# Performance work log

Measured on AMD Instinct MI355X. Metric: run time of the kernel, lower is better.

The kernel has to match this reference:

```python
import jax, jax.numpy as jnp
import numpy as np

N_NODES = 20000
N_EDGES = 320000
N_FEAT = 128
MLP_HID = 64
N_GRAPHS = 16
N_LAYERS = 5
EPS = 1e-5


def setup_inputs() -> dict:
    key = jax.random.key(0)
    ks = jax.random.split(key, 8)
    x = jax.random.normal(ks[0], (N_NODES, N_FEAT), dtype=jnp.float32)
    edge_index = jax.random.randint(ks[1], (2, N_EDGES), 0, N_NODES, dtype=jnp.int64)
    batch = jnp.sort(jax.random.randint(ks[2], (N_NODES,), 0, N_GRAPHS, dtype=jnp.int64))
    W1 = jax.random.normal(ks[3], (N_LAYERS, N_FEAT, MLP_HID), dtype=jnp.float32) * 0.05
    b1 = jnp.zeros((N_LAYERS, MLP_HID), dtype=jnp.float32)
    W2 = jax.random.normal(ks[4], (N_LAYERS, MLP_HID, N_FEAT), dtype=jnp.float32) * 0.05
    b2 = jnp.zeros((N_LAYERS, N_FEAT), dtype=jnp.float32)
    gn_weight = jnp.ones((N_LAYERS, N_FEAT), dtype=jnp.float32)
    gn_bias = jnp.zeros((N_LAYERS, N_FEAT), dtype=jnp.float32)
    gn_scale = jnp.ones((N_LAYERS, N_FEAT), dtype=jnp.float32)
    lin_w = jax.random.normal(ks[5], (N_FEAT, 1), dtype=jnp.float32) * 0.05
    lin_b = jnp.zeros((1,), dtype=jnp.float32)
    return {"x": x, "edge_index": edge_index, "batch": batch,
            "W1": W1, "b1": b1, "W2": W2, "b2": b2,
            "gn_weight": gn_weight, "gn_bias": gn_bias, "gn_scale": gn_scale,
            "lin_w": lin_w, "lin_b": lin_b}


def _conv(h, src, dst, W1, b1, W2, b2):
    # message MLP is per-source-node, so compute MLP(x) once per node,
    # then gather by src and scatter-add to dst. Self loops add m[i] at i.
    m = jax.nn.relu(h @ W1 + b1) @ W2 + b2  # [N, C]
    return jax.ops.segment_sum(m[src], dst, num_segments=N_NODES) + m


def _graph_norm(h, batch, cnt, w, b, a):
    mean = jax.ops.segment_sum(h, batch, num_segments=N_GRAPHS) / cnt  # [G, C]
    out = h - a * mean[batch]
    var = jax.ops.segment_sum(out * out, batch, num_segments=N_GRAPHS) / cnt
    out = out * jax.lax.rsqrt(var[batch] + EPS)
    return w * out + b


def reference(x, edge_index, batch, W1, b1, W2, b2, gn_weight, gn_bias, gn_scale, lin_w, lin_b):
    src, dst = edge_index[0], edge_index[1]
    cnt = jax.ops.segment_sum(jnp.ones((N_NODES, 1), x.dtype), batch,
                              num_segments=N_GRAPHS)
    cnt = jnp.maximum(cnt, 1.0)  # [G, 1]
    h = x
    for i in range(N_LAYERS):
        g = _conv(h, src, dst, W1[i], b1[i], W2[i], b2[i])
        g = _graph_norm(g, batch, cnt, gn_weight[i], gn_bias[i], gn_scale[i])
        g = jax.nn.relu(g)  # dropout is identity in eval mode
        h = g if i == 0 else g + h  # residual from layer 2 onward
    pooled = jax.ops.segment_sum(h, batch, num_segments=N_GRAPHS) / cnt  # [G, C]
    return pooled @ lin_w + lin_b  # [G, 1]
```

## Files before the change

### kernel.cpp

```cpp
#include <hip/hip_runtime.h>

#define N_NODES 20000
#define N_EDGES 320000
#define N_FEAT 128
#define MLP_HID 64
#define N_GRAPHS 16
#define N_LAYERS 5
#define EPS 1e-5f

typedef __attribute__((ext_vector_type(8))) short short8;
typedef __attribute__((ext_vector_type(4))) float f32x4;

__device__ inline float bf2f(unsigned short u) { return __uint_as_float(((unsigned)u) << 16); }
__device__ inline unsigned short f2bf(float f) {
  unsigned u = __float_as_uint(f);
  u += 0x7FFF + ((u >> 16) & 1);
  return (unsigned short)(u >> 16);
}


__global__ __launch_bounds__(256) void k_deg(const int* __restrict__ dst, int* __restrict__ deg) {
  int e = blockIdx.x * 256 + threadIdx.x;
  atomicAdd(&deg[dst[e]], 1);
}

__global__ __launch_bounds__(1024) void k_scan(const int* __restrict__ deg, int* __restrict__ rowptr,
                                               int* __restrict__ cursor, const int* __restrict__ batch,
                                               float* __restrict__ cntf, float* __restrict__ pooled) {
  __shared__ int sdata[1024];
  __shared__ int spos[17];
  constexpr int CH = 20;
  int t = threadIdx.x;
  for (int i = t; i < N_GRAPHS * N_FEAT; i += 1024) pooled[i] = 0.0f;
  int base = t * CH;
  int loc[CH];
  int partial = 0;
#pragma unroll
  for (int i = 0; i < CH; i++) {
    int idx = base + i;
    int v = (idx < N_NODES) ? deg[idx] : 0;
    loc[i] = v;
    partial += v;
  }
  sdata[t] = partial;
  __syncthreads();
  for (int off = 1; off < 1024; off <<= 1) {
    int v = (t >= off) ? sdata[t - off] : 0;
    __syncthreads();
    sdata[t] += v;
    __syncthreads();
  }
  int run = sdata[t] - partial;
#pragma unroll
  for (int i = 0; i < CH; i++) {
    int idx = base + i;
    if (idx < N_NODES) {
      rowptr[idx] = run;
      cursor[idx] = run;
      run += loc[i];
    }
  }
  if (t == 1023) rowptr[N_NODES] = sdata[1023];
  if (t < 17) {
    int lo = 0, hi = N_NODES;
    while (lo < hi) {
      int mid = (lo + hi) >> 1;
      if (batch[mid] < t) lo = mid + 1; else hi = mid;
    }
    spos[t] = lo;
  }
  __syncthreads();
  if (t < N_GRAPHS) cntf[t] = fmaxf((float)(spos[t + 1] - spos[t]), 1.0f);
}

__global__ __launch_bounds__(256) void k_fill(const int* __restrict__ src, const int* __restrict__ dst,
                                              int* __restrict__ cursor, unsigned short* __restrict__ src_sorted) {
  int e = blockIdx.x * 256 + threadIdx.x;
  int d = dst[e];
  int p = atomicAdd(&cursor[d], 1);
  src_sorted[p] = (unsigned short)src[e];
}


__global__ __launch_bounds__(256) void k_prep(const float* __restrict__ W1, const float* __restrict__ W2,
                                              unsigned short* __restrict__ w1t, unsigned short* __restrict__ w2t) {
  int idx = blockIdx.x * 256 + threadIdx.x;
  if (idx < 40960) {
    int l = idx >> 13, rem = idx & 8191;
    int n = rem >> 7, k = rem & 127;
    w1t[idx] = f2bf(W1[l * 8192 + k * 64 + n]);
  } else {
    int j = idx - 40960;
    int l = j >> 13, rem = j & 8191;
    int n = rem >> 6, k = rem & 63;
    w2t[j] = f2bf(W2[l * 8192 + k * 128 + n]);
  }
}


#define PADK 136
#define PADH 72

__global__ __launch_bounds__(256) void k_mlp(const float* __restrict__ hin, unsigned short* __restrict__ mout,
                                             const unsigned short* __restrict__ w1t,
                                             const unsigned short* __restrict__ w2t,
                                             const float* __restrict__ b1, const float* __restrict__ b2) {
  __shared__ __align__(16) short hS[64 * PADK];
  __shared__ __align__(16) short w1S[64 * PADK];
  __shared__ __align__(16) short hidS[64 * PADH];
  __shared__ __align__(16) short w2S[128 * PADH];
  __shared__ float b1S[64];
  __shared__ float b2S[128];
  int t = threadIdx.x;
  int r0 = blockIdx.x * 64;
#pragma unroll
  for (int i = 0; i < 8; i++) {
    int idx = t + i * 256;
    int row = idx >> 5, c4 = idx & 31;
    float4 v = (r0 + row < N_NODES) ? ((const float4*)hin)[(size_t)(r0 + row) * 32 + c4]
                                    : make_float4(0.f, 0.f, 0.f, 0.f);
    ushort4 s;
    s.x = f2bf(v.x); s.y = f2bf(v.y); s.z = f2bf(v.z); s.w = f2bf(v.w);
    *(ushort4*)&hS[row * PADK + c4 * 4] = s;
  }
#pragma unroll
  for (int i = 0; i < 4; i++) {
    int idx = t + i * 256;
    *(int4*)&w1S[(idx >> 4) * PADK + (idx & 15) * 8] = ((const int4*)w1t)[idx];
    *(int4*)&w2S[(idx >> 3) * PADH + (idx & 7) * 8] = ((const int4*)w2t)[idx];
  }
  if (t < 64) b1S[t] = b1[t];
  else if (t < 192) b2S[t - 64] = b2[t - 64];
  __syncthreads();

  int w = t >> 6, lane = t & 63, lm = lane & 15, quad = lane >> 4;
  int mrow = w * 16 + lm;
  int orow = w * 16 + quad * 4;

  f32x4 zero = {0.f, 0.f, 0.f, 0.f};
  f32x4 acc[4] = {zero, zero, zero, zero};
#pragma unroll
  for (int k0 = 0; k0 < 128; k0 += 32) {
    short8 a = *(const short8*)&hS[mrow * PADK + k0 + quad * 8];
#pragma unroll
    for (int nt = 0; nt < 4; nt++) {
      short8 b = *(const short8*)&w1S[(nt * 16 + lm) * PADK + k0 + quad * 8];
      acc[nt] = __builtin_amdgcn_mfma_f32_16x16x32_bf16(a, b, acc[nt], 0, 0, 0);
    }
  }
#pragma unroll
  for (int nt = 0; nt < 4; nt++) {
    int col = nt * 16 + lm;
    float bb = b1S[col];
#pragma unroll
    for (int r = 0; r < 4; r++)
      hidS[(orow + r) * PADH + col] = (short)f2bf(fmaxf(acc[nt][r] + bb, 0.0f));
  }
  __syncthreads();

  f32x4 acc2[8] = {zero, zero, zero, zero, zero, zero, zero, zero};
#pragma unroll
  for (int k0 = 0; k0 < 64; k0 += 32) {
    short8 a = *(const short8*)&hidS[mrow * PADH + k0 + quad * 8];
#pragma unroll
    for (int nt = 0; nt < 8; nt++) {
      short8 b = *(const short8*)&w2S[(nt * 16 + lm) * PADH + k0 + quad * 8];
      acc2[nt] = __builtin_amdgcn_mfma_f32_16x16x32_bf16(a, b, acc2[nt], 0, 0, 0);
    }
  }
#pragma unroll
  for (int nt = 0; nt < 8; nt++) {
    int col = nt * 16 + lm;
    float bb = b2S[col];
#pragma unroll
    for (int r = 0; r < 4; r++)
      hS[(orow + r) * PADK + col] = (short)f2bf(acc2[nt][r] + bb);
  }
  __syncthreads();
#pragma unroll
  for (int i = 0; i < 4; i++) {
    int idx = t + i * 256;
    int row = idx >> 4, cc = idx & 15;
    if (r0 + row < N_NODES)
      ((int4*)mout)[(size_t)(r0 + row) * 16 + cc] = *(const int4*)&hS[row * PADK + cc * 8];
  }
}


__global__ __launch_bounds__(256) void k_scatter(const unsigned short* __restrict__ mbf, float* __restrict__ g,
                                                 const int* __restrict__ rowptr,
                                                 const unsigned short* __restrict__ srcs,
                                                 float* __restrict__ s1, float* __restrict__ s2) {
  if (blockIdx.x == 0) {
    for (int i = threadIdx.x; i < N_GRAPHS * N_FEAT; i += 256) { s1[i] = 0.0f; s2[i] = 0.0f; }
  }
  int node = (blockIdx.x * 256 + threadIdx.x) >> 6;
  int lane = threadIdx.x & 63;
  int quarter = lane >> 4;
  int q16 = lane & 15;
  const float4* m4 = (const float4*)mbf;
  float acc[8];
  union BU { float4 f; unsigned short u[8]; };
  if (quarter == 0) {
    BU U; U.f = m4[(size_t)node * 16 + q16];
#pragma unroll
    for (int j = 0; j < 8; j++) acc[j] = bf2f(U.u[j]);
  } else {
#pragma unroll
    for (int j = 0; j < 8; j++) acc[j] = 0.0f;
  }
  int e = rowptr[node], e1 = rowptr[node + 1];
  for (; e + 16 <= e1; e += 16) {
    int i0 = srcs[e + quarter];
    int i1 = srcs[e + 4 + quarter];
    int i2 = srcs[e + 8 + quarter];
    int i3 = srcs[e + 12 + quarter];
    BU U0, U1, U2, U3;
    U0.f = m4[(size_t)i0 * 16 + q16];
    U1.f = m4[(size_t)i1 * 16 + q16];
    U2.f = m4[(size_t)i2 * 16 + q16];
    U3.f = m4[(size_t)i3 * 16 + q16];
#pragma unroll
    for (int j = 0; j < 8; j++)
      acc[j] += (bf2f(U0.u[j]) + bf2f(U1.u[j])) + (bf2f(U2.u[j]) + bf2f(U3.u[j]));
  }
  for (; e + 4 <= e1; e += 4) {
    BU U0; U0.f = m4[(size_t)srcs[e + quarter] * 16 + q16];
#pragma unroll
    for (int j = 0; j < 8; j++) acc[j] += bf2f(U0.u[j]);
  }
  if (e + quarter < e1) {
    BU U0; U0.f = m4[(size_t)srcs[e + quarter] * 16 + q16];
#pragma unroll
    for (int j = 0; j < 8; j++) acc[j] += bf2f(U0.u[j]);
  }
#pragma unroll
  for (int j = 0; j < 8; j++) {
    acc[j] += __shfl_xor(acc[j], 16);
    acc[j] += __shfl_xor(acc[j], 32);
  }
  if (quarter == 0) {
    float4* g4 = (float4*)(g + (size_t)node * 128 + q16 * 8);
    g4[0] = make_float4(acc[0], acc[1], acc[2], acc[3]);
    g4[1] = make_float4(acc[4], acc[5], acc[6], acc[7]);
  }
}


#define STAT_CHUNK 8

__global__ __launch_bounds__(128) void k_stats(const float* __restrict__ in, const int* __restrict__ batch,
                                               float* __restrict__ s1, float* __restrict__ s2) {
  int n0 = blockIdx.x * STAT_CHUNK;
  int c = threadIdx.x;
  int curg = batch[n0];
  float a1 = 0.0f, a2 = 0.0f;
#pragma unroll
  for (int k = 0; k < STAT_CHUNK; k++) {
    int n = n0 + k;
    int gg = batch[n];
    if (gg != curg) {
      atomicAdd(&s1[curg * 128 + c], a1);
      atomicAdd(&s2[curg * 128 + c], a2);
      a1 = 0.0f; a2 = 0.0f;
      curg = gg;
    }
    float v = in[(size_t)n * 128 + c];
    a1 += v;
    a2 += v * v;
  }
  atomicAdd(&s1[curg * 128 + c], a1);
  atomicAdd(&s2[curg * 128 + c], a2);
}

__global__ __launch_bounds__(128) void k_segsum(const float* __restrict__ in, const int* __restrict__ batch,
                                                float* __restrict__ outbuf) {
  int n0 = blockIdx.x * STAT_CHUNK;
  int c = threadIdx.x;
  int curg = batch[n0];
  float acc = 0.0f;
#pragma unroll
  for (int k = 0; k < STAT_CHUNK; k++) {
    int n = n0 + k;
    int gg = batch[n];
    if (gg != curg) {
      atomicAdd(&outbuf[curg * 128 + c], acc);
      acc = 0.0f;
      curg = gg;
    }
    acc += in[(size_t)n * 128 + c];
  }
  atomicAdd(&outbuf[curg * 128 + c], acc);
}


__global__ __launch_bounds__(256) void k_apply(const float* __restrict__ gin, float* __restrict__ h,
                                               const int* __restrict__ batch,
                                               const float* __restrict__ s1, const float* __restrict__ s2,
                                               const float* __restrict__ cntf,
                                               const float* __restrict__ w, const float* __restrict__ b,
                                               const float* __restrict__ a, int residual) {
  int idx = blockIdx.x * 256 + threadIdx.x;
  int n = idx >> 5, c4 = idx & 31;
  int gg = batch[n];
  float invc = 1.0f / cntf[gg];
  float4 sm = ((const float4*)s1)[gg * 32 + c4];
  float4 se = ((const float4*)s2)[gg * 32 + c4];
  float4 av = ((const float4*)a)[c4];
  float4 wv = ((const float4*)w)[c4];
  float4 bv = ((const float4*)b)[c4];
  float4 gv = ((const float4*)gin)[idx];
  float4 hv = make_float4(0.f, 0.f, 0.f, 0.f);
  if (residual) hv = ((const float4*)h)[idx];
  float4 o;
#define APPLY1(X)                                                          \
  {                                                                        \
    float mean = sm.X * invc;                                              \
    float ex2 = se.X * invc;                                               \
    float ac = av.X;                                                       \
    float var = fmaxf(ex2 - mean * mean * (2.0f * ac - ac * ac), 0.0f);    \
    float d = gv.X - ac * mean;                                            \
    float y = wv.X * (d * rsqrtf(var + EPS)) + bv.X;                       \
    y = fmaxf(y, 0.0f);                                                    \
    o.X = residual ? (y + hv.X) : y;                                       \
  }
  APPLY1(x) APPLY1(y) APPLY1(z) APPLY1(w)
#undef APPLY1
  ((float4*)h)[idx] = o;
}


__global__ __launch_bounds__(256) void k_final(const float* __restrict__ pooled, const float* __restrict__ cntf,
                                               const float* __restrict__ lw, const float* __restrict__ lb,
                                               float* __restrict__ out) {
  int lane = threadIdx.x & 63, wave = threadIdx.x >> 6;
  for (int gi = 0; gi < 4; gi++) {
    int gidx = wave * 4 + gi;
    float s = pooled[gidx * 128 + lane] * lw[lane] + pooled[gidx * 128 + 64 + lane] * lw[64 + lane];
    for (int o = 32; o >= 1; o >>= 1) s += __shfl_down(s, o);
    if (lane == 0) out[gidx] = s / cntf[gidx] + lb[0];
  }
}


extern "C" void kernel_launch(void* const* d_in, const int* in_sizes, int n_in,
                              void* d_out, int out_size, void* d_ws, size_t ws_size,
                              hipStream_t stream) {
  const float* x = (const float*)d_in[0];
  const int* ei = (const int*)d_in[1];
  const int* batch = (const int*)d_in[2];
  const float* W1 = (const float*)d_in[3];
  const float* b1 = (const float*)d_in[4];
  const float* W2 = (const float*)d_in[5];
  const float* b2 = (const float*)d_in[6];
  const float* gnw = (const float*)d_in[7];
  const float* gnb = (const float*)d_in[8];
  const float* gna = (const float*)d_in[9];
  const float* lw = (const float*)d_in[10];
  const float* lb = (const float*)d_in[11];
  float* out = (float*)d_out;

  const int* srcI = ei;
  const int* dstI = ei + N_EDGES;

  char* p = (char*)d_ws;
  float* hbuf = (float*)(p + 0);
  unsigned short* mbuf = (unsigned short*)(p + 10240000);
  float* gbuf = (float*)(p + 20480000);
  unsigned short* src_sorted = (unsigned short*)(p + 30720000);
  int* rowptr = (int*)(p + 32000000);
  int* cursor = (int*)(p + 32080128);
  int* deg = (int*)(p + 32160256);
  float* cntf = (float*)(p + 32240512);
  float* s1buf = (float*)(p + 32240640);
  float* s2buf = (float*)(p + 32248832);
  float* pooled = (float*)(p + 32257024);
  unsigned short* w1t = (unsigned short*)(p + 32265216);
  unsigned short* w2t = (unsigned short*)(p + 32347136);

  hipMemsetAsync(deg, 0, N_NODES * sizeof(int), stream);
  k_deg<<<N_EDGES / 256, 256, 0, stream>>>(dstI, deg);
  k_scan<<<1, 1024, 0, stream>>>(deg, rowptr, cursor, batch, cntf, pooled);
  k_fill<<<N_EDGES / 256, 256, 0, stream>>>(srcI, dstI, cursor, src_sorted);
  k_prep<<<320, 256, 0, stream>>>(W1, W2, w1t, w2t);

  const float* hin = x;
  for (int i = 0; i < N_LAYERS; i++) {
    k_mlp<<<(N_NODES + 63) / 64, 256, 0, stream>>>(hin, mbuf, w1t + (size_t)i * 8192, w2t + (size_t)i * 8192,
                                                   b1 + (size_t)i * 64, b2 + (size_t)i * 128);
    k_scatter<<<N_NODES / 4, 256, 0, stream>>>(mbuf, gbuf, rowptr, src_sorted, s1buf, s2buf);
    k_stats<<<N_NODES / STAT_CHUNK, 128, 0, stream>>>(gbuf, batch, s1buf, s2buf);
    k_apply<<<N_NODES * N_FEAT / 4 / 256, 256, 0, stream>>>(gbuf, hbuf, batch, s1buf, s2buf, cntf,
                                                            gnw + (size_t)i * 128, gnb + (size_t)i * 128,
                                                            gna + (size_t)i * 128, i > 0 ? 1 : 0);
    hin = hbuf;
  }

  k_segsum<<<N_NODES / STAT_CHUNK, 128, 0, stream>>>(hbuf, batch, pooled);
  k_final<<<1, 256, 0, stream>>>(pooled, cntf, lw, lb, out);
}
```

Baseline: 336.2 us.

## Fuse setup kernels and fold final pooling into last graph-norm apply

Merges the degree count, scan and weight-prep kernels into one setup launch. The degree histogram now uses shared-memory atomics inside the single scan block, which removes a memset and a global-atomic kernel. The last layer's normalize/residual kernel also accumulates the per-graph pooled sums through shared memory and atomics, so the separate segment-sum pass over h is gone. The cost is a serial single-block degree count over all edges and some extra atomics in the final apply.

```diff
diff --git a/kernel.cpp b/kernel.cpp
--- a/kernel.cpp
+++ b/kernel.cpp
@@ -19,26 +19,42 @@
 }
 
 
-__global__ __launch_bounds__(256) void k_deg(const int* __restrict__ dst, int* __restrict__ deg) {
-  int e = blockIdx.x * 256 + threadIdx.x;
-  atomicAdd(&deg[dst[e]], 1);
-}
-
-__global__ __launch_bounds__(1024) void k_scan(const int* __restrict__ deg, int* __restrict__ rowptr,
-                                               int* __restrict__ cursor, const int* __restrict__ batch,
-                                               float* __restrict__ cntf, float* __restrict__ pooled) {
+__global__ __launch_bounds__(1024) void k_setup(const float* __restrict__ W1, const float* __restrict__ W2,
+                                                unsigned short* __restrict__ w1t, unsigned short* __restrict__ w2t,
+                                                const int* __restrict__ dst, const int* __restrict__ batch,
+                                                int* __restrict__ rowptr, int* __restrict__ cursor,
+                                                float* __restrict__ cntf, float* __restrict__ pooled) {
+  __shared__ int degS[N_NODES];
   __shared__ int sdata[1024];
   __shared__ int spos[17];
+  int t = threadIdx.x;
+  if (blockIdx.x < 80) {
+    int idx = blockIdx.x * 1024 + t;
+    if (idx < 40960) {
+      int l = idx >> 13, rem = idx & 8191;
+      int n = rem >> 7, k = rem & 127;
+      w1t[idx] = f2bf(W1[l * 8192 + k * 64 + n]);
+    } else {
+      int j = idx - 40960;
+      int l = j >> 13, rem = j & 8191;
+      int n = rem >> 6, k = rem & 63;
+      w2t[j] = f2bf(W2[l * 8192 + k * 128 + n]);
+    }
+    return;
+  }
+  for (int i = t; i < N_NODES; i += 1024) degS[i] = 0;
+  for (int i = t; i < N_GRAPHS * N_FEAT; i += 1024) pooled[i] = 0.0f;
+  __syncthreads();
+  for (int i = t; i < N_EDGES; i += 1024) atomicAdd(&degS[dst[i]], 1);
+  __syncthreads();
   constexpr int CH = 20;
-  int t = threadIdx.x;
-  for (int i = t; i < N_GRAPHS * N_FEAT; i += 1024) pooled[i] = 0.0f;
   int base = t * CH;
   int loc[CH];
   int partial = 0;
 #pragma unroll
   for (int i = 0; i < CH; i++) {
     int idx = base + i;
-    int v = (idx < N_NODES) ? deg[idx] : 0;
+    int v = (idx < N_NODES) ? degS[idx] : 0;
     loc[i] = v;
     partial += v;
   }
@@ -79,22 +95,6 @@
   int d = dst[e];
   int p = atomicAdd(&cursor[d], 1);
   src_sorted[p] = (unsigned short)src[e];
-}
-
-
-__global__ __launch_bounds__(256) void k_prep(const float* __restrict__ W1, const float* __restrict__ W2,
-                                              unsigned short* __restrict__ w1t, unsigned short* __restrict__ w2t) {
-  int idx = blockIdx.x * 256 + threadIdx.x;
-  if (idx < 40960) {
-    int l = idx >> 13, rem = idx & 8191;
-    int n = rem >> 7, k = rem & 127;
-    w1t[idx] = f2bf(W1[l * 8192 + k * 64 + n]);
-  } else {
-    int j = idx - 40960;
-    int l = j >> 13, rem = j & 8191;
-    int n = rem >> 6, k = rem & 63;
-    w2t[j] = f2bf(W2[l * 8192 + k * 128 + n]);
-  }
 }
 
 
@@ -271,26 +271,6 @@
   }
   atomicAdd(&s1[curg * 128 + c], a1);
   atomicAdd(&s2[curg * 128 + c], a2);
-}
-
-__global__ __launch_bounds__(128) void k_segsum(const float* __restrict__ in, const int* __restrict__ batch,
-                                                float* __restrict__ outbuf) {
-  int n0 = blockIdx.x * STAT_CHUNK;
-  int c = threadIdx.x;
-  int curg = batch[n0];
-  float acc = 0.0f;
-#pragma unroll
-  for (int k = 0; k < STAT_CHUNK; k++) {
-    int n = n0 + k;
-    int gg = batch[n];
-    if (gg != curg) {
-      atomicAdd(&outbuf[curg * 128 + c], acc);
-      acc = 0.0f;
-      curg = gg;
-    }
-    acc += in[(size_t)n * 128 + c];
-  }
-  atomicAdd(&outbuf[curg * 128 + c], acc);
 }
 
 
@@ -330,6 +310,58 @@
 }
 
 
+__global__ __launch_bounds__(256) void k_apply_pool(const float* __restrict__ gin, const float* __restrict__ h,
+                                                    const int* __restrict__ batch,
+                                                    const float* __restrict__ s1, const float* __restrict__ s2,
+                                                    const float* __restrict__ cntf,
+                                                    const float* __restrict__ gw, const float* __restrict__ gb,
+                                                    const float* __restrict__ ga,
+                                                    float* __restrict__ pooled) {
+  __shared__ float pS[8][128];
+  int t = threadIdx.x;
+  int idx = blockIdx.x * 256 + t;
+  int n = idx >> 5, c4 = idx & 31;
+  int gg = batch[n];
+  float invc = 1.0f / cntf[gg];
+  float4 sm = ((const float4*)s1)[gg * 32 + c4];
+  float4 se = ((const float4*)s2)[gg * 32 + c4];
+  float4 av = ((const float4*)ga)[c4];
+  float4 wv = ((const float4*)gw)[c4];
+  float4 bv = ((const float4*)gb)[c4];
+  float4 gv = ((const float4*)gin)[idx];
+  float4 hv = ((const float4*)h)[idx];
+  float4 o;
+#define APPLY1(X)                                                          \
+  {                                                                        \
+    float mean = sm.X * invc;                                              \
+    float ex2 = se.X * invc;                                               \
+    float ac = av.X;                                                       \
+    float var = fmaxf(ex2 - mean * mean * (2.0f * ac - ac * ac), 0.0f);    \
+    float d = gv.X - ac * mean;                                            \
+    float y = wv.X * (d * rsqrtf(var + EPS)) + bv.X;                       \
+    y = fmaxf(y, 0.0f);                                                    \
+    o.X = y + hv.X;                                                        \
+  }
+  APPLY1(x) APPLY1(y) APPLY1(z) APPLY1(w)
+#undef APPLY1
+  *(float4*)&pS[t >> 5][c4 * 4] = o;
+  __syncthreads();
+  int n0 = blockIdx.x * 8;
+  int gA = batch[n0], gB = batch[n0 + 7];
+  if (t < 128) {
+    if (gA == gB) {
+      float s = 0.f;
+#pragma unroll
+      for (int ww = 0; ww < 8; ww++) s += pS[ww][t];
+      atomicAdd(&pooled[gA * 128 + t], s);
+    } else {
+#pragma unroll
+      for (int ww = 0; ww < 8; ww++) atomicAdd(&pooled[batch[n0 + ww] * 128 + t], pS[ww][t]);
+    }
+  }
+}
+
+
 __global__ __launch_bounds__(256) void k_final(const float* __restrict__ pooled, const float* __restrict__ cntf,
                                                const float* __restrict__ lw, const float* __restrict__ lb,
                                                float* __restrict__ out) {
@@ -370,7 +402,6 @@
   unsigned short* src_sorted = (unsigned short*)(p + 30720000);
   int* rowptr = (int*)(p + 32000000);
   int* cursor = (int*)(p + 32080128);
-  int* deg = (int*)(p + 32160256);
   float* cntf = (float*)(p + 32240512);
   float* s1buf = (float*)(p + 32240640);
   float* s2buf = (float*)(p + 32248832);
@@ -378,11 +409,8 @@
   unsigned short* w1t = (unsigned short*)(p + 32265216);
   unsigned short* w2t = (unsigned short*)(p + 32347136);
 
-  hipMemsetAsync(deg, 0, N_NODES * sizeof(int), stream);
-  k_deg<<<N_EDGES / 256, 256, 0, stream>>>(dstI, deg);
-  k_scan<<<1, 1024, 0, stream>>>(deg, rowptr, cursor, batch, cntf, pooled);
+  k_setup<<<81, 1024, 0, stream>>>(W1, W2, w1t, w2t, dstI, batch, rowptr, cursor, cntf, pooled);
   k_fill<<<N_EDGES / 256, 256, 0, stream>>>(srcI, dstI, cursor, src_sorted);
-  k_prep<<<320, 256, 0, stream>>>(W1, W2, w1t, w2t);
 
   const float* hin = x;
   for (int i = 0; i < N_LAYERS; i++) {
@@ -390,12 +418,17 @@
                                                    b1 + (size_t)i * 64, b2 + (size_t)i * 128);
     k_scatter<<<N_NODES / 4, 256, 0, stream>>>(mbuf, gbuf, rowptr, src_sorted, s1buf, s2buf);
     k_stats<<<N_NODES / STAT_CHUNK, 128, 0, stream>>>(gbuf, batch, s1buf, s2buf);
-    k_apply<<<N_NODES * N_FEAT / 4 / 256, 256, 0, stream>>>(gbuf, hbuf, batch, s1buf, s2buf, cntf,
-                                                            gnw + (size_t)i * 128, gnb + (size_t)i * 128,
-                                                            gna + (size_t)i * 128, i > 0 ? 1 : 0);
-    hin = hbuf;
-  }
-
-  k_segsum<<<N_NODES / STAT_CHUNK, 128, 0, stream>>>(hbuf, batch, pooled);
+    if (i < N_LAYERS - 1) {
+      k_apply<<<N_NODES * N_FEAT / 4 / 256, 256, 0, stream>>>(gbuf, hbuf, batch, s1buf, s2buf, cntf,
+                                                              gnw + (size_t)i * 128, gnb + (size_t)i * 128,
+                                                              gna + (size_t)i * 128, i > 0 ? 1 : 0);
+      hin = hbuf;
+    } else {
+      k_apply_pool<<<N_NODES / 8, 256, 0, stream>>>(gbuf, hbuf, batch, s1buf, s2buf, cntf,
+                                                    gnw + (size_t)i * 128, gnb + (size_t)i * 128,
+                                                    gna + (size_t)i * 128, pooled);
+    }
+  }
+
   k_final<<<1, 256, 0, stream>>>(pooled, cntf, lw, lb, out);
 }
```

After: 391.2 us. 1.16x slower.
